# Kernel tuning notes

Measured on AMD Instinct MI355X. Metric: run time of the kernel, lower is better.

## Reference

```python
import jax, jax.numpy as jnp
import numpy as np

B, S, D = 8, 1024, 768
H, DH = 12, 64
FF = 3072
E = 8
CAP = 2 * (B * S) // E  # capacity per expert; routing of randn inputs never exceeds this
EPS = 1e-12


def layer_norm(x, g, b):
    mu = jnp.mean(x, axis=-1, keepdims=True)
    var = jnp.var(x, axis=-1, keepdims=True)
    return (x - mu) * jax.lax.rsqrt(var + EPS) * g + b


def setup_inputs() -> dict:
    key = jax.random.key(0)
    ks = jax.random.split(key, 16)
    sd = 0.02
    inp = {
        "hidden_states": jax.random.normal(ks[0], (B, S, D), jnp.float32),
        "attention_mask": jnp.zeros((B, 1, 1, S), jnp.float32),
        "Wq": jax.random.normal(ks[1], (D, D), jnp.float32) * sd,
        "bq": jnp.zeros((D,), jnp.float32),
        "Wk": jax.random.normal(ks[2], (D, D), jnp.float32) * sd,
        "bk": jnp.zeros((D,), jnp.float32),
        "Wv": jax.random.normal(ks[3], (D, D), jnp.float32) * sd,
        "bv": jnp.zeros((D,), jnp.float32),
        "Wo": jax.random.normal(ks[4], (D, D), jnp.float32) * sd,
        "bo": jnp.zeros((D,), jnp.float32),
        "ln1_g": jnp.ones((D,), jnp.float32),
        "ln1_b": jnp.zeros((D,), jnp.float32),
        "Wr": jax.random.normal(ks[5], (D, E), jnp.float32) * sd,
        "br": jnp.zeros((E,), jnp.float32),
        "W1": jax.random.normal(ks[6], (E, D, FF), jnp.float32) * sd,
        "b1": jnp.zeros((E, FF), jnp.float32),
        "W2": jax.random.normal(ks[7], (E, FF, D), jnp.float32) * sd,
        "b2": jnp.zeros((E, D), jnp.float32),
        "ln2_g": jnp.ones((D,), jnp.float32),
        "ln2_b": jnp.zeros((D,), jnp.float32),
    }
    return inp


def reference(hidden_states, attention_mask, Wq, bq, Wk, bk, Wv, bv, Wo, bo,
              ln1_g, ln1_b, Wr, br, W1, b1, W2, b2, ln2_g, ln2_b):
    x = hidden_states
    # ---- BERT self-attention (post-norm inside Attention) ----
    def heads(t):  # [B,S,D] -> [B,H,S,DH]
        return t.reshape(B, S, H, DH).transpose(0, 2, 1, 3)
    q = heads(x @ Wq + bq)
    k = heads(x @ Wk + bk)
    v = heads(x @ Wv + bv)
    scores = jnp.einsum('bhsd,bhtd->bhst', q, k) / jnp.sqrt(jnp.float32(DH))
    scores = scores + attention_mask  # additive mask, broadcast [B,1,1,S]
    probs = jax.nn.softmax(scores, axis=-1)
    ctx = jnp.einsum('bhst,bhtd->bhsd', probs, v)
    ctx = ctx.transpose(0, 2, 1, 3).reshape(B, S, D)
    att_output = layer_norm(x + (ctx @ Wo + bo), ln1_g, ln1_b)

    # ---- Switch (top-1) MoE FFN ----
    T = B * S
    xf = att_output.reshape(T, D)
    route = jax.nn.softmax(xf @ Wr + br, axis=-1)      # [T,E]
    gate = jnp.max(route, axis=-1)                      # [T]
    eidx = jnp.argmax(route, axis=-1)                   # [T]
    oh = jax.nn.one_hot(eidx, E, dtype=jnp.int32)       # [T,E]
    pos = (jnp.cumsum(oh, axis=0) * oh).sum(-1) - 1     # position within expert
    keep = (pos < CAP).astype(xf.dtype)                 # capacity drop mask
    p = jnp.clip(pos, 0, CAP - 1)
    # scatter tokens into per-expert buffers [E,CAP,D]
    buf = jnp.zeros((E, CAP, D), xf.dtype).at[eidx, p].add(xf * keep[:, None])
    h = jax.nn.gelu(jnp.einsum('ecd,edf->ecf', buf, W1) + b1[:, None, :], approximate=False)
    y = jnp.einsum('ecf,efd->ecd', h, W2) + b2[:, None, :]
    ffn = y[eidx, p] * (keep * gate)[:, None]            # gather + scale by route prob
    ffn_output = ffn.reshape(B, S, D)

    # dropout p=0 -> identity; post-norm residual
    return layer_norm(att_output + ffn_output, ln2_g, ln2_b)
```

## Files before the change

kernel.cpp:

```cpp
#include <hip/hip_runtime.h>
#include <hip/hip_bf16.h>
#include <math.h>

#define B_ 8
#define S_ 1024
#define D_ 768
#define H_ 12
#define DH_ 64
#define FF_ 3072
#define E_ 8
#define CAP_ 2048
#define T_ (B_ * S_)
#define QKVSTR 2304
#define QKSTR 1536

typedef __bf16 bf16_t;
typedef bf16_t bf16x8_t __attribute__((ext_vector_type(8)));
typedef bf16_t bf16x4_t __attribute__((ext_vector_type(4)));
typedef float floatx4_t __attribute__((ext_vector_type(4)));
typedef _Float16 f16_t;
typedef f16_t f16x8_t __attribute__((ext_vector_type(8)));
typedef f16_t f16x4_t __attribute__((ext_vector_type(4)));

#define LSTR 40

__global__ __launch_bounds__(256) void mfma_gemm_kernel(
    const bf16_t* __restrict__ Abase, const bf16_t* __restrict__ Btbase,
    const float* __restrict__ biasbase, bf16_t* __restrict__ Cbase,
    const int* __restrict__ cnt, int cnt_off,
    int M, int N, int K,
    long strideAz, long strideBz, long strideBiasz, long strideCz,
    int apply_gelu)
{
    __shared__ bf16_t As[128 * LSTR];
    __shared__ bf16_t Bs[128 * LSTR];
    const int z = blockIdx.z;
    const int row0 = blockIdx.y * 128;
    const int col0 = blockIdx.x * 128;
    if (cnt && row0 >= cnt[cnt_off + z]) return;
    const bf16_t* A  = Abase + (size_t)z * strideAz;
    const bf16_t* Bt = Btbase + (size_t)z * strideBz;
    const float* bias = biasbase + (size_t)z * strideBiasz;
    bf16_t* C = Cbase + (size_t)z * strideCz;

    const int tid = threadIdx.x;
    const int lane = tid & 63, wave = tid >> 6;
    const int wm = (wave >> 1) * 64, wn = (wave & 1) * 64;
    const int l16 = lane & 15, quad = lane >> 4;

    floatx4_t acc[4][4] = {};

    const int ch0 = tid, ch1 = tid + 256;
    const int r0a = ch0 >> 2, kc0 = (ch0 & 3) * 8;
    const int r1a = ch1 >> 2, kc1 = (ch1 & 3) * 8;

    for (int k0 = 0; k0 < K; k0 += 32) {
        __syncthreads();
        *(int4*)&As[r0a * LSTR + kc0] = *(const int4*)&A[(size_t)(row0 + r0a) * K + k0 + kc0];
        *(int4*)&As[r1a * LSTR + kc1] = *(const int4*)&A[(size_t)(row0 + r1a) * K + k0 + kc1];
        *(int4*)&Bs[r0a * LSTR + kc0] = *(const int4*)&Bt[(size_t)(col0 + r0a) * K + k0 + kc0];
        *(int4*)&Bs[r1a * LSTR + kc1] = *(const int4*)&Bt[(size_t)(col0 + r1a) * K + k0 + kc1];
        __syncthreads();
        bf16x8_t a[4], b[4];
        #pragma unroll
        for (int mt = 0; mt < 4; mt++)
            a[mt] = *(bf16x8_t*)&As[(wm + mt * 16 + l16) * LSTR + quad * 8];
        #pragma unroll
        for (int nt = 0; nt < 4; nt++)
            b[nt] = *(bf16x8_t*)&Bs[(wn + nt * 16 + l16) * LSTR + quad * 8];
        #pragma unroll
        for (int mt = 0; mt < 4; mt++)
            #pragma unroll
            for (int nt = 0; nt < 4; nt++)
                acc[mt][nt] = __builtin_amdgcn_mfma_f32_16x16x32_bf16(a[mt], b[nt], acc[mt][nt], 0, 0, 0);
    }

    #pragma unroll
    for (int mt = 0; mt < 4; mt++) {
        #pragma unroll
        for (int nt = 0; nt < 4; nt++) {
            const int col = col0 + wn + nt * 16 + l16;
            const float bv = bias[col];
            #pragma unroll
            for (int r = 0; r < 4; r++) {
                const int row = row0 + wm + mt * 16 + quad * 4 + r;
                float v = acc[mt][nt][r] + bv;
                if (apply_gelu) v = 0.5f * v * (1.0f + erff(v * 0.70710678118654752f));
                C[(size_t)row * N + col] = (bf16_t)v;
            }
        }
    }
}

__global__ __launch_bounds__(256) void mfma_split_gemm_kernel(
    const f16_t* __restrict__ Ah, const f16_t* __restrict__ Al,
    const f16_t* __restrict__ Bth, const f16_t* __restrict__ Btl,
    const float* __restrict__ bias0, const float* __restrict__ bias1,
    const float* __restrict__ bias2,
    float* __restrict__ C, int K, int N, int mode,
    f16_t* __restrict__ qkh, f16_t* __restrict__ qkl,
    f16_t* __restrict__ vth, f16_t* __restrict__ vtl)
{
    __shared__ f16_t Ash[128 * LSTR], Asl[128 * LSTR];
    __shared__ f16_t Bsh[128 * LSTR], Bsl[128 * LSTR];
    const int row0 = blockIdx.y * 128;
    const int col0 = blockIdx.x * 128;

    const int tid = threadIdx.x;
    const int lane = tid & 63, wave = tid >> 6;
    const int wm = (wave >> 1) * 64, wn = (wave & 1) * 64;
    const int l16 = lane & 15, quad = lane >> 4;

    floatx4_t acc[4][4] = {};

    const int r0a = tid >> 2, kc0 = (tid & 3) * 8;
    const int r1a = r0a + 64;

    for (int k0 = 0; k0 < K; k0 += 32) {
        __syncthreads();
        const size_t a0 = (size_t)(row0 + r0a) * K + k0 + kc0;
        const size_t a1 = (size_t)(row0 + r1a) * K + k0 + kc0;
        const size_t b0 = (size_t)(col0 + r0a) * K + k0 + kc0;
        const size_t b1 = (size_t)(col0 + r1a) * K + k0 + kc0;
        *(int4*)&Ash[r0a * LSTR + kc0] = *(const int4*)&Ah[a0];
        *(int4*)&Ash[r1a * LSTR + kc0] = *(const int4*)&Ah[a1];
        *(int4*)&Asl[r0a * LSTR + kc0] = *(const int4*)&Al[a0];
        *(int4*)&Asl[r1a * LSTR + kc0] = *(const int4*)&Al[a1];
        *(int4*)&Bsh[r0a * LSTR + kc0] = *(const int4*)&Bth[b0];
        *(int4*)&Bsh[r1a * LSTR + kc0] = *(const int4*)&Bth[b1];
        *(int4*)&Bsl[r0a * LSTR + kc0] = *(const int4*)&Btl[b0];
        *(int4*)&Bsl[r1a * LSTR + kc0] = *(const int4*)&Btl[b1];
        __syncthreads();
        f16x8_t bh[4], bl[4];
        #pragma unroll
        for (int nt = 0; nt < 4; nt++) {
            bh[nt] = *(f16x8_t*)&Bsh[(wn + nt * 16 + l16) * LSTR + quad * 8];
            bl[nt] = *(f16x8_t*)&Bsl[(wn + nt * 16 + l16) * LSTR + quad * 8];
        }
        #pragma unroll
        for (int mt = 0; mt < 4; mt++) {
            f16x8_t ah = *(f16x8_t*)&Ash[(wm + mt * 16 + l16) * LSTR + quad * 8];
            f16x8_t al = *(f16x8_t*)&Asl[(wm + mt * 16 + l16) * LSTR + quad * 8];
            #pragma unroll
            for (int nt = 0; nt < 4; nt++) {
                acc[mt][nt] = __builtin_amdgcn_mfma_f32_16x16x32_f16(ah, bh[nt], acc[mt][nt], 0, 0, 0);
                acc[mt][nt] = __builtin_amdgcn_mfma_f32_16x16x32_f16(al, bh[nt], acc[mt][nt], 0, 0, 0);
                acc[mt][nt] = __builtin_amdgcn_mfma_f32_16x16x32_f16(ah, bl[nt], acc[mt][nt], 0, 0, 0);
            }
        }
    }

    const int wsel = col0 / 768;
    const float* bias = (wsel == 0) ? bias0 : (wsel == 1) ? bias1 : bias2;
    const int colsub = col0 % 768;

    if (mode == 1) {
        if (col0 < 1536) {
            #pragma unroll
            for (int mt = 0; mt < 4; mt++) {
                #pragma unroll
                for (int nt = 0; nt < 4; nt++) {
                    const int col = col0 + wn + nt * 16 + l16;
                    const float bv = bias[colsub + wn + nt * 16 + l16];
                    #pragma unroll
                    for (int r = 0; r < 4; r++) {
                        const int row = row0 + wm + mt * 16 + quad * 4 + r;
                        float v = acc[mt][nt][r] * (1.0f / 64.0f) + bv;
                        f16_t hh = (f16_t)v;
                        const size_t o = (size_t)row * QKSTR + col;
                        qkh[o] = hh; qkl[o] = (f16_t)(v - (float)hh);
                    }
                }
            }
        } else {
            #pragma unroll
            for (int mt = 0; mt < 4; mt++) {
                const int rowb = row0 + wm + mt * 16 + quad * 4;
                const int bb = rowb >> 10, ss = rowb & 1023;
                #pragma unroll
                for (int nt = 0; nt < 4; nt++) {
                    const int d = (col0 - 1536) + wn + nt * 16 + l16;
                    const int hidx = d >> 6, dd = d & 63;
                    const float bv = bias[colsub + wn + nt * 16 + l16];
                    f16x4_t hv, lv;
                    #pragma unroll
                    for (int r = 0; r < 4; r++) {
                        float v = acc[mt][nt][r] * (1.0f / 64.0f) + bv;
                        hv[r] = (f16_t)v; lv[r] = (f16_t)(v - (float)hv[r]);
                    }
                    const size_t o = ((size_t)(bb * H_ + hidx) * DH_ + dd) * S_ + ss;
                    *(f16x4_t*)&vth[o] = hv;
                    *(f16x4_t*)&vtl[o] = lv;
                }
            }
        }
    } else {
        #pragma unroll
        for (int mt = 0; mt < 4; mt++) {
            #pragma unroll
            for (int nt = 0; nt < 4; nt++) {
                const int col = col0 + wn + nt * 16 + l16;
                const float bv = bias[colsub + wn + nt * 16 + l16];
                #pragma unroll
                for (int r = 0; r < 4; r++) {
                    const int row = row0 + wm + mt * 16 + quad * 4 + r;
                    C[(size_t)row * N + col] = acc[mt][nt][r] * (1.0f / 64.0f) + bv;
                }
            }
        }
    }
}

__global__ __launch_bounds__(256) void cast_split_kernel(
    const float* __restrict__ src, f16_t* __restrict__ hi, f16_t* __restrict__ lo)
{
    const int i = blockIdx.x * 256 + threadIdx.x;
    float4 v = ((const float4*)src)[i];
    const float vv[4] = {v.x, v.y, v.z, v.w};
    f16x4_t h, l;
    #pragma unroll
    for (int c = 0; c < 4; c++) {
        f16_t hh = (f16_t)vv[c];
        h[c] = hh; l[c] = (f16_t)(vv[c] - (float)hh);
    }
    ((f16x4_t*)hi)[i] = h;
    ((f16x4_t*)lo)[i] = l;
}

__global__ __launch_bounds__(256) void transpose_cast_split_kernel(
    const float* __restrict__ src, f16_t* __restrict__ dsth, f16_t* __restrict__ dstl,
    int R, int C)
{
    __shared__ float tile[32][33];
    const int r0 = blockIdx.y * 32, c0 = blockIdx.x * 32;
    const int tid = threadIdx.x;
    const int tr = tid >> 3, tc4 = (tid & 7) * 4;
    float4 v = *(const float4*)&src[(size_t)(r0 + tr) * C + c0 + tc4];
    tile[tr][tc4 + 0] = v.x * 64.0f; tile[tr][tc4 + 1] = v.y * 64.0f;
    tile[tr][tc4 + 2] = v.z * 64.0f; tile[tr][tc4 + 3] = v.w * 64.0f;
    __syncthreads();
    const int cc = tid >> 3, rr4 = (tid & 7) * 4;
    f16x4_t h, l;
    #pragma unroll
    for (int i = 0; i < 4; i++) {
        float f = tile[rr4 + i][cc];
        f16_t hh = (f16_t)f;
        h[i] = hh; l[i] = (f16_t)(f - (float)hh);
    }
    *(f16x4_t*)&dsth[(size_t)(c0 + cc) * R + r0 + rr4] = h;
    *(f16x4_t*)&dstl[(size_t)(c0 + cc) * R + r0 + rr4] = l;
}

__global__ __launch_bounds__(256) void transpose_cast_kernel(
    const float* __restrict__ src, bf16_t* __restrict__ dst, int R, int C)
{
    __shared__ float tile[32][33];
    const size_t zoff = (size_t)blockIdx.z * R * C;
    const float* s = src + zoff;
    bf16_t* d = dst + zoff;
    const int r0 = blockIdx.y * 32, c0 = blockIdx.x * 32;
    const int tid = threadIdx.x;
    const int tr = tid >> 3, tc4 = (tid & 7) * 4;
    float4 v = *(const float4*)&s[(size_t)(r0 + tr) * C + c0 + tc4];
    tile[tr][tc4 + 0] = v.x; tile[tr][tc4 + 1] = v.y;
    tile[tr][tc4 + 2] = v.z; tile[tr][tc4 + 3] = v.w;
    __syncthreads();
    const int cc = tid >> 3, rr4 = (tid & 7) * 4;
    bf16x4_t o;
    #pragma unroll
    for (int i = 0; i < 4; i++) o[i] = (bf16_t)tile[rr4 + i][cc];
    *(bf16x4_t*)&d[(size_t)(c0 + cc) * R + r0 + rr4] = o;
}

#define FSTR 72

__global__ __launch_bounds__(256) void flash_attn_mfma_kernel(
    const f16_t* __restrict__ qkh, const f16_t* __restrict__ qkl,
    const f16_t* __restrict__ vth, const f16_t* __restrict__ vtl,
    const float* __restrict__ mask,
    f16_t* __restrict__ ctxh, f16_t* __restrict__ ctxl)
{
    __shared__ f16_t Kh[64 * FSTR], Kl[64 * FSTR];
    __shared__ f16_t Vh[64 * FSTR], Vl[64 * FSTR];
    __shared__ f16_t Ph[64 * FSTR], Pl[64 * FSTR];
    const int flat = blockIdx.x;
    const int qt = (flat >> 3) & 15;
    const int p  = (flat & 7) + 8 * (flat >> 7);
    const int h = p % H_, b = p / H_;
    const int tid = threadIdx.x;
    const int lane = tid & 63, wave = tid >> 6;
    const int l16 = lane & 15, quad = lane >> 4;
    const int wm = wave * 16;
    const int q0 = qt * 64;
    const int pswz_w = quad << 3;
    const int quadr = quad ^ ((l16 >> 2) & 3);

    const size_t qoff = (size_t)(b * S_ + q0 + wm + l16) * QKSTR + h * DH_ + quad * 8;
    f16x8_t qh[2], ql[2];
    qh[0] = *(const f16x8_t*)&qkh[qoff];
    qh[1] = *(const f16x8_t*)&qkh[qoff + 32];
    ql[0] = *(const f16x8_t*)&qkl[qoff];
    ql[1] = *(const f16x8_t*)&qkl[qoff + 32];

    const int r0 = tid >> 3, s0 = (tid & 7) * 8;
    const int r1 = r0 + 32, s1 = s0;
    const size_t kbase = (size_t)b * S_ * QKSTR + 768 + (size_t)h * DH_;
    const size_t vbase = (size_t)(b * H_ + h) * DH_ * (size_t)S_;

    int4 kr0h, kr1h, kr0l, kr1l, vr0h, vr1h, vr0l, vr1l;
    auto prefetch = [&](int k0) {
        kr0h = *(const int4*)&qkh[kbase + (size_t)(k0 + r0) * QKSTR + s0];
        kr1h = *(const int4*)&qkh[kbase + (size_t)(k0 + r1) * QKSTR + s1];
        kr0l = *(const int4*)&qkl[kbase + (size_t)(k0 + r0) * QKSTR + s0];
        kr1l = *(const int4*)&qkl[kbase + (size_t)(k0 + r1) * QKSTR + s1];
        vr0h = *(const int4*)&vth[vbase + (size_t)r0 * S_ + k0 + s0];
        vr1h = *(const int4*)&vth[vbase + (size_t)r1 * S_ + k0 + s1];
        vr0l = *(const int4*)&vtl[vbase + (size_t)r0 * S_ + k0 + s0];
        vr1l = *(const int4*)&vtl[vbase + (size_t)r1 * S_ + k0 + s1];
    };
    prefetch(0);

    floatx4_t Oacc[4] = {};
    float mrun[4], lrun[4];
    #pragma unroll
    for (int i = 0; i < 4; i++) { mrun[i] = -1e30f; lrun[i] = 0.f; }

    for (int kt = 0; kt < S_ / 64; kt++) {
        __syncthreads();
        *(int4*)&Kh[r0 * FSTR + s0] = kr0h;
        *(int4*)&Kh[r1 * FSTR + s1] = kr1h;
        *(int4*)&Kl[r0 * FSTR + s0] = kr0l;
        *(int4*)&Kl[r1 * FSTR + s1] = kr1l;
        *(int4*)&Vh[r0 * FSTR + s0] = vr0h;
        *(int4*)&Vh[r1 * FSTR + s1] = vr1h;
        *(int4*)&Vl[r0 * FSTR + s0] = vr0l;
        *(int4*)&Vl[r1 * FSTR + s1] = vr1l;
        __syncthreads();
        if (kt + 1 < S_ / 64) prefetch((kt + 1) * 64);

        floatx4_t sacc[4] = {};
        __builtin_amdgcn_s_setprio(1);
        #pragma unroll
        for (int ks2 = 0; ks2 < 2; ks2++) {
            const f16x8_t ah = qh[ks2], al = ql[ks2];
            #pragma unroll
            for (int nt = 0; nt < 4; nt++) {
                f16x8_t bh = *(f16x8_t*)&Kh[(nt * 16 + l16) * FSTR + ks2 * 32 + quad * 8];
                f16x8_t bl = *(f16x8_t*)&Kl[(nt * 16 + l16) * FSTR + ks2 * 32 + quad * 8];
                sacc[nt] = __builtin_amdgcn_mfma_f32_16x16x32_f16(ah, bh, sacc[nt], 0, 0, 0);
                sacc[nt] = __builtin_amdgcn_mfma_f32_16x16x32_f16(al, bh, sacc[nt], 0, 0, 0);
                sacc[nt] = __builtin_amdgcn_mfma_f32_16x16x32_f16(ah, bl, sacc[nt], 0, 0, 0);
            }
        }
        __builtin_amdgcn_s_setprio(0);

        const int k0 = kt * 64;
        float mk[4];
        #pragma unroll
        for (int nt = 0; nt < 4; nt++) mk[nt] = mask[b * S_ + k0 + nt * 16 + l16];

        #pragma unroll
        for (int r = 0; r < 4; r++) {
            float s[4];
            float rmax = -1e30f;
            #pragma unroll
            for (int nt = 0; nt < 4; nt++) {
                s[nt] = sacc[nt][r] * 0.125f + mk[nt];
                rmax = fmaxf(rmax, s[nt]);
            }
            #pragma unroll
            for (int off = 1; off < 16; off <<= 1) rmax = fmaxf(rmax, __shfl_xor(rmax, off));
            if (rmax > mrun[r]) {
                const float alpha = __expf(mrun[r] - rmax);
                mrun[r] = rmax;
                lrun[r] *= alpha;
                #pragma unroll
                for (int nt = 0; nt < 4; nt++) Oacc[nt][r] *= alpha;
            }
            const float mnew = mrun[r];
            const int row = wm + quad * 4 + r;
            float rsum = 0.f;
            #pragma unroll
            for (int nt = 0; nt < 4; nt++) {
                float pv = __expf(s[nt] - mnew);
                f16_t ph = (f16_t)pv;
                const int csw = (nt * 16 + l16) ^ pswz_w;
                Ph[row * FSTR + csw] = ph;
                Pl[row * FSTR + csw] = (f16_t)(pv - (float)ph);
                rsum += pv;
            }
            #pragma unroll
            for (int off = 1; off < 16; off <<= 1) rsum += __shfl_xor(rsum, off);
            lrun[r] += rsum;
        }

        __builtin_amdgcn_s_setprio(1);
        #pragma unroll
        for (int ks2 = 0; ks2 < 2; ks2++) {
            f16x8_t ah = *(f16x8_t*)&Ph[(wm + l16) * FSTR + ks2 * 32 + quadr * 8];
            f16x8_t al = *(f16x8_t*)&Pl[(wm + l16) * FSTR + ks2 * 32 + quadr * 8];
            #pragma unroll
            for (int nt = 0; nt < 4; nt++) {
                f16x8_t bh = *(f16x8_t*)&Vh[(nt * 16 + l16) * FSTR + ks2 * 32 + quad * 8];
                f16x8_t bl = *(f16x8_t*)&Vl[(nt * 16 + l16) * FSTR + ks2 * 32 + quad * 8];
                Oacc[nt] = __builtin_amdgcn_mfma_f32_16x16x32_f16(ah, bh, Oacc[nt], 0, 0, 0);
                Oacc[nt] = __builtin_amdgcn_mfma_f32_16x16x32_f16(al, bh, Oacc[nt], 0, 0, 0);
                Oacc[nt] = __builtin_amdgcn_mfma_f32_16x16x32_f16(ah, bl, Oacc[nt], 0, 0, 0);
            }
        }
        __builtin_amdgcn_s_setprio(0);
    }

    float invl[4];
    #pragma unroll
    for (int r = 0; r < 4; r++) invl[r] = 1.0f / lrun[r];
    #pragma unroll
    for (int nt = 0; nt < 4; nt++) {
        #pragma unroll
        for (int r = 0; r < 4; r++) {
            const float v = Oacc[nt][r] * invl[r];
            const f16_t hh = (f16_t)v;
            const size_t o = (size_t)(b * S_ + q0 + wm + quad * 4 + r) * D_ + h * DH_ + nt * 16 + l16;
            ctxh[o] = hh;
            ctxl[o] = (f16_t)(v - (float)hh);
        }
    }
}

__global__ __launch_bounds__(256) void add_ln_kernel(
    const float* __restrict__ x, const float* __restrict__ y,
    const float* __restrict__ g, const float* __restrict__ bb,
    float* __restrict__ out)
{
    const int t = blockIdx.x;
    const int tid = threadIdx.x;
    __shared__ float red[256];
    float vals[3];
    float lsum = 0.f;
    #pragma unroll
    for (int i = 0; i < 3; i++) {
        int c = tid + i * 256;
        float v = x[(size_t)t * D_ + c] + y[(size_t)t * D_ + c];
        vals[i] = v; lsum += v;
    }
    red[tid] = lsum; __syncthreads();
    for (int off = 128; off > 0; off >>= 1) { if (tid < off) red[tid] += red[tid + off]; __syncthreads(); }
    const float mu = red[0] * (1.0f / D_);
    __syncthreads();
    float lvar = 0.f;
    #pragma unroll
    for (int i = 0; i < 3; i++) { float d = vals[i] - mu; lvar += d * d; }
    red[tid] = lvar; __syncthreads();
    for (int off = 128; off > 0; off >>= 1) { if (tid < off) red[tid] += red[tid + off]; __syncthreads(); }
    const float rstd = rsqrtf(red[0] * (1.0f / D_) + 1e-12f);
    #pragma unroll
    for (int i = 0; i < 3; i++) {
        int c = tid + i * 256;
        out[(size_t)t * D_ + c] = (vals[i] - mu) * rstd * g[c] + bb[c];
    }
}

__global__ __launch_bounds__(64) void router_kernel(
    const float* __restrict__ att, const float* __restrict__ Wr,
    const float* __restrict__ br, float* __restrict__ gate, int* __restrict__ eidx)
{
    const int t = blockIdx.x;
    const int lane = threadIdx.x;
    float lg[E_] = {};
    for (int d = lane; d < D_; d += 64) {
        float xv = att[(size_t)t * D_ + d];
        #pragma unroll
        for (int e = 0; e < E_; e++) lg[e] += xv * Wr[d * E_ + e];
    }
    #pragma unroll
    for (int off = 32; off > 0; off >>= 1)
        #pragma unroll
        for (int e = 0; e < E_; e++) lg[e] += __shfl_down(lg[e], off);
    if (lane == 0) {
        float mx = -1e30f; int mi = 0;
        #pragma unroll
        for (int e = 0; e < E_; e++) {
            lg[e] += br[e];
            if (lg[e] > mx) { mx = lg[e]; mi = e; }
        }
        float ssum = 0.f;
        #pragma unroll
        for (int e = 0; e < E_; e++) ssum += expf(lg[e] - mx);
        gate[t] = 1.0f / ssum;
        eidx[t] = mi;
    }
}

__global__ __launch_bounds__(256) void pos_scan_kernel(
    const int* __restrict__ eidx, const float* __restrict__ gate,
    int* __restrict__ pos, float* __restrict__ scale, int* __restrict__ cnt_out)
{
    __shared__ int cnt[256][E_];
    const int tid = threadIdx.x;
    const int start = tid * (T_ / 256);
    int lc[E_] = {};
    for (int i = 0; i < T_ / 256; i++) lc[eidx[start + i]]++;
    #pragma unroll
    for (int e = 0; e < E_; e++) cnt[tid][e] = lc[e];
    __syncthreads();
    if (tid < E_) {
        int run = 0;
        for (int i = 0; i < 256; i++) { int c = cnt[i][tid]; cnt[i][tid] = run; run += c; }
        cnt_out[tid] = run;
    }
    __syncthreads();
    int off[E_];
    #pragma unroll
    for (int e = 0; e < E_; e++) off[e] = cnt[tid][e];
    for (int i = 0; i < T_ / 256; i++) {
        int tk = start + i;
        int e = eidx[tk];
        int p = off[e]++;
        bool keep = p < CAP_;
        pos[tk] = p < CAP_ - 1 ? p : CAP_ - 1;
        scale[tk] = keep ? gate[tk] : 0.0f;
    }
}

__global__ __launch_bounds__(256) void scatter_kernel(
    const float* __restrict__ att, const int* __restrict__ eidx,
    const int* __restrict__ pos, const float* __restrict__ scale,
    bf16_t* __restrict__ buf)
{
    const int t = blockIdx.x;
    if (scale[t] == 0.0f) return;
    const int tid = threadIdx.x;
    const float* src = att + (size_t)t * D_;
    bf16_t* dst = buf + ((size_t)eidx[t] * CAP_ + pos[t]) * D_;
    for (int i = tid; i < D_; i += 256) dst[i] = (bf16_t)src[i];
}

__global__ __launch_bounds__(256) void final_ln_kernel(
    const float* __restrict__ att, const bf16_t* __restrict__ y,
    const int* __restrict__ eidx, const int* __restrict__ pos,
    const float* __restrict__ scale,
    const float* __restrict__ g, const float* __restrict__ bb,
    float* __restrict__ out)
{
    const int t = blockIdx.x;
    const int tid = threadIdx.x;
    __shared__ float red[256];
    const float sc = scale[t];
    const bf16_t* yrow = y + ((size_t)eidx[t] * CAP_ + pos[t]) * D_;
    float vals[3];
    float lsum = 0.f;
    #pragma unroll
    for (int i = 0; i < 3; i++) {
        int c = tid + i * 256;
        float v = att[(size_t)t * D_ + c] + (float)yrow[c] * sc;
        vals[i] = v; lsum += v;
    }
    red[tid] = lsum; __syncthreads();
    for (int off = 128; off > 0; off >>= 1) { if (tid < off) red[tid] += red[tid + off]; __syncthreads(); }
    const float mu = red[0] * (1.0f / D_);
    __syncthreads();
    float lvar = 0.f;
    #pragma unroll
    for (int i = 0; i < 3; i++) { float d = vals[i] - mu; lvar += d * d; }
    red[tid] = lvar; __syncthreads();
    for (int off = 128; off > 0; off >>= 1) { if (tid < off) red[tid] += red[tid + off]; __syncthreads(); }
    const float rstd = rsqrtf(red[0] * (1.0f / D_) + 1e-12f);
    #pragma unroll
    for (int i = 0; i < 3; i++) {
        int c = tid + i * 256;
        out[(size_t)t * D_ + c] = (vals[i] - mu) * rstd * g[c] + bb[c];
    }
}

extern "C" void kernel_launch(void* const* d_in, const int* in_sizes, int n_in,
                              void* d_out, int out_size, void* d_ws, size_t ws_size,
                              hipStream_t stream) {
    const float* x     = (const float*)d_in[0];
    const float* mask  = (const float*)d_in[1];
    const float* Wq    = (const float*)d_in[2];
    const float* bq    = (const float*)d_in[3];
    const float* Wk    = (const float*)d_in[4];
    const float* bk    = (const float*)d_in[5];
    const float* Wv    = (const float*)d_in[6];
    const float* bv    = (const float*)d_in[7];
    const float* Wo    = (const float*)d_in[8];
    const float* bo    = (const float*)d_in[9];
    const float* ln1g  = (const float*)d_in[10];
    const float* ln1b  = (const float*)d_in[11];
    const float* Wr    = (const float*)d_in[12];
    const float* br    = (const float*)d_in[13];
    const float* W1    = (const float*)d_in[14];
    const float* b1    = (const float*)d_in[15];
    const float* W2    = (const float*)d_in[16];
    const float* b2    = (const float*)d_in[17];
    const float* ln2g  = (const float*)d_in[18];
    const float* ln2b  = (const float*)d_in[19];
    float* out = (float*)d_out;

    char* ws = (char*)d_ws;
    const size_t TDB = (size_t)T_ * D_ * 4;
    f16_t* qkh  = (f16_t*)(ws);
    f16_t* qkl  = (f16_t*)(ws + TDB);
    f16_t* vth  = (f16_t*)(ws + 2 * TDB);
    f16_t* vtl  = (f16_t*)(ws + 2 * TDB + TDB / 2);
    f16_t* ctxh = (f16_t*)(ws + 3 * TDB);
    f16_t* ctxl = (f16_t*)(ws + 3 * TDB + TDB / 2);
    float* att_buf = (float*)(ws + 4 * TDB);
    f16_t* xh = (f16_t*)(ws + 3 * TDB);
    f16_t* xl = xh + (size_t)T_ * D_;
    f16_t* wqkvT_h = (f16_t*)(ws + 4 * TDB);
    f16_t* wqkvT_l = wqkvT_h + (size_t)QKVSTR * D_;
    f16_t* woT_h   = wqkvT_l + (size_t)QKVSTR * D_;
    f16_t* woT_l   = woT_h + (size_t)D_ * D_;
    float* proj_b = (float*)(ws);
    bf16_t* W1T = (bf16_t*)(ws);
    bf16_t* W2T = (bf16_t*)(ws + (size_t)E_ * FF_ * D_ * 2);
    bf16_t* h_b = (bf16_t*)(ws + (size_t)2 * E_ * FF_ * D_ * 2);
    char*  smallp  = ws + 5 * TDB;
    float* gate_b  = (float*)(smallp);
    int*   eidx_b  = (int*)(smallp + 32768);
    int*   pos_b   = (int*)(smallp + 2 * 32768);
    float* scale_b = (float*)(smallp + 3 * 32768);
    int*   cnt_b   = (int*)(smallp + 4 * 32768);
    bf16_t* buf_b  = (bf16_t*)(smallp + 4 * 32768 + 128);
    bf16_t* y_b    = (bf16_t*)((char*)buf_b + (size_t)E_ * CAP_ * D_ * 2);
    bf16_t* h8_b   = (bf16_t*)((char*)y_b + (size_t)E_ * CAP_ * D_ * 2);
    const size_t need8 = ((char*)h8_b - ws) + (size_t)E_ * CAP_ * FF_ * 2;

    dim3 blk(256);
    cast_split_kernel<<<dim3(T_ * D_ / 1024), blk, 0, stream>>>(x, xh, xl);
    transpose_cast_split_kernel<<<dim3(D_ / 32, D_ / 32), blk, 0, stream>>>(
        Wq, wqkvT_h, wqkvT_l, D_, D_);
    transpose_cast_split_kernel<<<dim3(D_ / 32, D_ / 32), blk, 0, stream>>>(
        Wk, wqkvT_h + (size_t)D_ * D_, wqkvT_l + (size_t)D_ * D_, D_, D_);
    transpose_cast_split_kernel<<<dim3(D_ / 32, D_ / 32), blk, 0, stream>>>(
        Wv, wqkvT_h + (size_t)2 * D_ * D_, wqkvT_l + (size_t)2 * D_ * D_, D_, D_);
    transpose_cast_split_kernel<<<dim3(D_ / 32, D_ / 32), blk, 0, stream>>>(
        Wo, woT_h, woT_l, D_, D_);
    mfma_split_gemm_kernel<<<dim3(QKVSTR / 128, T_ / 128), blk, 0, stream>>>(
        xh, xl, wqkvT_h, wqkvT_l, bq, bk, bv, nullptr, D_, QKVSTR,
        1, qkh, qkl, vth, vtl);
    flash_attn_mfma_kernel<<<dim3((S_ / 64) * H_ * B_), blk, 0, stream>>>(
        qkh, qkl, vth, vtl, mask, ctxh, ctxl);
    mfma_split_gemm_kernel<<<dim3(D_ / 128, T_ / 128), blk, 0, stream>>>(
        ctxh, ctxl, woT_h, woT_l, bo, bo, bo, proj_b, D_, D_,
        0, nullptr, nullptr, nullptr, nullptr);
    add_ln_kernel<<<dim3(T_), blk, 0, stream>>>(x, proj_b, ln1g, ln1b, att_buf);
    router_kernel<<<dim3(T_), dim3(64), 0, stream>>>(att_buf, Wr, br, gate_b, eidx_b);
    pos_scan_kernel<<<dim3(1), blk, 0, stream>>>(eidx_b, gate_b, pos_b, scale_b, cnt_b);
    transpose_cast_kernel<<<dim3(FF_ / 32, D_ / 32, E_), blk, 0, stream>>>(W1, W1T, D_, FF_);
    transpose_cast_kernel<<<dim3(D_ / 32, FF_ / 32, E_), blk, 0, stream>>>(W2, W2T, FF_, D_);
    hipMemsetAsync(buf_b, 0, (size_t)E_ * CAP_ * D_ * 2, stream);
    scatter_kernel<<<dim3(T_), blk, 0, stream>>>(att_buf, eidx_b, pos_b, scale_b, buf_b);
    if (ws_size >= need8) {
        mfma_gemm_kernel<<<dim3(FF_ / 128, CAP_ / 128, E_), blk, 0, stream>>>(
            buf_b, W1T, b1, h8_b,
            cnt_b, 0, CAP_, FF_, D_,
            (long)CAP_ * D_, (long)FF_ * D_, (long)FF_, (long)CAP_ * FF_, 1);
        mfma_gemm_kernel<<<dim3(D_ / 128, CAP_ / 128, E_), blk, 0, stream>>>(
            h8_b, W2T, b2, y_b,
            cnt_b, 0, CAP_, D_, FF_,
            (long)CAP_ * FF_, (long)D_ * FF_, (long)D_, (long)CAP_ * D_, 0);
    } else {
        for (int bch = 0; bch < 4; bch++) {
            const int e0 = bch * 2;
            mfma_gemm_kernel<<<dim3(FF_ / 128, CAP_ / 128, 2), blk, 0, stream>>>(
                buf_b + (size_t)e0 * CAP_ * D_, W1T + (size_t)e0 * FF_ * D_,
                b1 + (size_t)e0 * FF_, h_b,
                cnt_b, e0, CAP_, FF_, D_,
                (long)CAP_ * D_, (long)FF_ * D_, (long)FF_, (long)CAP_ * FF_, 1);
            mfma_gemm_kernel<<<dim3(D_ / 128, CAP_ / 128, 2), blk, 0, stream>>>(
                h_b, W2T + (size_t)e0 * D_ * FF_,
                b2 + (size_t)e0 * D_, y_b + (size_t)e0 * CAP_ * D_,
                cnt_b, e0, CAP_, D_, FF_,
                (long)CAP_ * FF_, (long)D_ * FF_, (long)D_, (long)CAP_ * D_, 0);
        }
    }
    final_ln_kernel<<<dim3(T_), blk, 0, stream>>>(att_buf, y_b, eidx_b, pos_b, scale_b, ln2g, ln2b, out);
}
```

Measured before the change: 842.7 us.

## Halve flash-attention KV tile to 32 keys and raise occupancy

```diff
diff --git a/kernel.cpp b/kernel.cpp
--- a/kernel.cpp
+++ b/kernel.cpp
@@ -272,17 +272,20 @@
     *(bf16x4_t*)&d[(size_t)(c0 + cc) * R + r0 + rr4] = o;
 }
 
-#define FSTR 72
-
-__global__ __launch_bounds__(256) void flash_attn_mfma_kernel(
+#define KVB 32
+#define KSTR 72
+#define VSTR 40
+#define PSTR 40
+
+__global__ __launch_bounds__(256, 5) void flash_attn_mfma_kernel(
     const f16_t* __restrict__ qkh, const f16_t* __restrict__ qkl,
     const f16_t* __restrict__ vth, const f16_t* __restrict__ vtl,
     const float* __restrict__ mask,
     f16_t* __restrict__ ctxh, f16_t* __restrict__ ctxl)
 {
-    __shared__ f16_t Kh[64 * FSTR], Kl[64 * FSTR];
-    __shared__ f16_t Vh[64 * FSTR], Vl[64 * FSTR];
-    __shared__ f16_t Ph[64 * FSTR], Pl[64 * FSTR];
+    __shared__ f16_t Kh[KVB * KSTR], Kl[KVB * KSTR];
+    __shared__ f16_t Vh[DH_ * VSTR], Vl[DH_ * VSTR];
+    __shared__ f16_t Ph[64 * PSTR],  Pl[64 * PSTR];
     const int flat = blockIdx.x;
     const int qt = (flat >> 3) & 15;
     const int p  = (flat & 7) + 8 * (flat >> 7);
@@ -292,8 +295,6 @@
     const int l16 = lane & 15, quad = lane >> 4;
     const int wm = wave * 16;
     const int q0 = qt * 64;
-    const int pswz_w = quad << 3;
-    const int quadr = quad ^ ((l16 >> 2) & 3);
 
     const size_t qoff = (size_t)(b * S_ + q0 + wm + l16) * QKSTR + h * DH_ + quad * 8;
     f16x8_t qh[2], ql[2];
@@ -302,21 +303,24 @@
     ql[0] = *(const f16x8_t*)&qkl[qoff];
     ql[1] = *(const f16x8_t*)&qkl[qoff + 32];
 
-    const int r0 = tid >> 3, s0 = (tid & 7) * 8;
-    const int r1 = r0 + 32, s1 = s0;
+    const int stv = tid >> 7;
+    const int t7 = tid & 127;
+    const int krow = t7 >> 2, kcol = (t7 & 3) * 16;
+    const int vrow = t7 >> 1, vcol = (t7 & 1) * 16;
     const size_t kbase = (size_t)b * S_ * QKSTR + 768 + (size_t)h * DH_;
     const size_t vbase = (size_t)(b * H_ + h) * DH_ * (size_t)S_;
 
-    int4 kr0h, kr1h, kr0l, kr1l, vr0h, vr1h, vr0l, vr1l;
+    int4 pr0h, pr1h, pr0l, pr1l;
     auto prefetch = [&](int k0) {
-        kr0h = *(const int4*)&qkh[kbase + (size_t)(k0 + r0) * QKSTR + s0];
-        kr1h = *(const int4*)&qkh[kbase + (size_t)(k0 + r1) * QKSTR + s1];
-        kr0l = *(const int4*)&qkl[kbase + (size_t)(k0 + r0) * QKSTR + s0];
-        kr1l = *(const int4*)&qkl[kbase + (size_t)(k0 + r1) * QKSTR + s1];
-        vr0h = *(const int4*)&vth[vbase + (size_t)r0 * S_ + k0 + s0];
-        vr1h = *(const int4*)&vth[vbase + (size_t)r1 * S_ + k0 + s1];
-        vr0l = *(const int4*)&vtl[vbase + (size_t)r0 * S_ + k0 + s0];
-        vr1l = *(const int4*)&vtl[vbase + (size_t)r1 * S_ + k0 + s1];
+        if (stv == 0) {
+            const size_t g = kbase + (size_t)(k0 + krow) * QKSTR + kcol;
+            pr0h = *(const int4*)&qkh[g]; pr1h = *(const int4*)&qkh[g + 8];
+            pr0l = *(const int4*)&qkl[g]; pr1l = *(const int4*)&qkl[g + 8];
+        } else {
+            const size_t g = vbase + (size_t)vrow * S_ + k0 + vcol;
+            pr0h = *(const int4*)&vth[g]; pr1h = *(const int4*)&vth[g + 8];
+            pr0l = *(const int4*)&vtl[g]; pr1l = *(const int4*)&vtl[g + 8];
+        }
     };
     prefetch(0);
 
@@ -325,28 +329,31 @@
     #pragma unroll
     for (int i = 0; i < 4; i++) { mrun[i] = -1e30f; lrun[i] = 0.f; }
 
-    for (int kt = 0; kt < S_ / 64; kt++) {
+    for (int kt = 0; kt < S_ / KVB; kt++) {
         __syncthreads();
-        *(int4*)&Kh[r0 * FSTR + s0] = kr0h;
-        *(int4*)&Kh[r1 * FSTR + s1] = kr1h;
-        *(int4*)&Kl[r0 * FSTR + s0] = kr0l;
-        *(int4*)&Kl[r1 * FSTR + s1] = kr1l;
-        *(int4*)&Vh[r0 * FSTR + s0] = vr0h;
-        *(int4*)&Vh[r1 * FSTR + s1] = vr1h;
-        *(int4*)&Vl[r0 * FSTR + s0] = vr0l;
-        *(int4*)&Vl[r1 * FSTR + s1] = vr1l;
+        if (stv == 0) {
+            f16_t* dh_ = &Kh[krow * KSTR + kcol];
+            f16_t* dl_ = &Kl[krow * KSTR + kcol];
+            *(int4*)dh_ = pr0h; *(int4*)(dh_ + 8) = pr1h;
+            *(int4*)dl_ = pr0l; *(int4*)(dl_ + 8) = pr1l;
+        } else {
+            f16_t* dh_ = &Vh[vrow * VSTR + vcol];
+            f16_t* dl_ = &Vl[vrow * VSTR + vcol];
+            *(int4*)dh_ = pr0h; *(int4*)(dh_ + 8) = pr1h;
+            *(int4*)dl_ = pr0l; *(int4*)(dl_ + 8) = pr1l;
+        }
         __syncthreads();
-        if (kt + 1 < S_ / 64) prefetch((kt + 1) * 64);
-
-        floatx4_t sacc[4] = {};
+        if (kt + 1 < S_ / KVB) prefetch((kt + 1) * KVB);
+
+        floatx4_t sacc[2] = {};
         __builtin_amdgcn_s_setprio(1);
         #pragma unroll
         for (int ks2 = 0; ks2 < 2; ks2++) {
             const f16x8_t ah = qh[ks2], al = ql[ks2];
             #pragma unroll
-            for (int nt = 0; nt < 4; nt++) {
-                f16x8_t bh = *(f16x8_t*)&Kh[(nt * 16 + l16) * FSTR + ks2 * 32 + quad * 8];
-                f16x8_t bl = *(f16x8_t*)&Kl[(nt * 16 + l16) * FSTR + ks2 * 32 + quad * 8];
+            for (int nt = 0; nt < 2; nt++) {
+                f16x8_t bh = *(f16x8_t*)&Kh[(nt * 16 + l16) * KSTR + ks2 * 32 + quad * 8];
+                f16x8_t bl = *(f16x8_t*)&Kl[(nt * 16 + l16) * KSTR + ks2 * 32 + quad * 8];
                 sacc[nt] = __builtin_amdgcn_mfma_f32_16x16x32_f16(ah, bh, sacc[nt], 0, 0, 0);
                 sacc[nt] = __builtin_amdgcn_mfma_f32_16x16x32_f16(al, bh, sacc[nt], 0, 0, 0);
                 sacc[nt] = __builtin_amdgcn_mfma_f32_16x16x32_f16(ah, bl, sacc[nt], 0, 0, 0);
@@ -354,59 +361,49 @@
         }
         __builtin_amdgcn_s_setprio(0);
 
-        const int k0 = kt * 64;
-        float mk[4];
-        #pragma unroll
-        for (int nt = 0; nt < 4; nt++) mk[nt] = mask[b * S_ + k0 + nt * 16 + l16];
+        const int k0 = kt * KVB;
+        float mk[2];
+        #pragma unroll
+        for (int nt = 0; nt < 2; nt++) mk[nt] = mask[b * S_ + k0 + nt * 16 + l16];
 
         #pragma unroll
         for (int r = 0; r < 4; r++) {
-            float s[4];
-            float rmax = -1e30f;
-            #pragma unroll
-            for (int nt = 0; nt < 4; nt++) {
-                s[nt] = sacc[nt][r] * 0.125f + mk[nt];
-                rmax = fmaxf(rmax, s[nt]);
+            float s0 = sacc[0][r] * 0.125f + mk[0];
+            float s1 = sacc[1][r] * 0.125f + mk[1];
+            float rmax = fmaxf(s0, s1);
+            #pragma unroll
+            for (int off = 1; off < 16; off <<= 1) rmax = fmaxf(rmax, __shfl_xor(rmax, off));
+            const float mnew = fmaxf(mrun[r], rmax);
+            const float alpha = __expf(mrun[r] - mnew);
+            mrun[r] = mnew;
+            const int row = wm + quad * 4 + r;
+            float p0 = __expf(s0 - mnew);
+            float p1 = __expf(s1 - mnew);
+            f16_t p0h = (f16_t)p0, p1h = (f16_t)p1;
+            Ph[row * PSTR + l16] = p0h;
+            Pl[row * PSTR + l16] = (f16_t)(p0 - (float)p0h);
+            Ph[row * PSTR + 16 + l16] = p1h;
+            Pl[row * PSTR + 16 + l16] = (f16_t)(p1 - (float)p1h);
+            float rsum = p0 + p1;
+            #pragma unroll
+            for (int off = 1; off < 16; off <<= 1) rsum += __shfl_xor(rsum, off);
+            lrun[r] = lrun[r] * alpha + rsum;
+            #pragma unroll
+            for (int nt2 = 0; nt2 < 4; nt2++) Oacc[nt2][r] *= alpha;
+        }
+
+        __builtin_amdgcn_s_setprio(1);
+        {
+            f16x8_t pah = *(f16x8_t*)&Ph[(wm + l16) * PSTR + quad * 8];
+            f16x8_t pal = *(f16x8_t*)&Pl[(wm + l16) * PSTR + quad * 8];
+            #pragma unroll
+            for (int nt2 = 0; nt2 < 4; nt2++) {
+                f16x8_t bh = *(f16x8_t*)&Vh[(nt2 * 16 + l16) * VSTR + quad * 8];
+                f16x8_t bl = *(f16x8_t*)&Vl[(nt2 * 16 + l16) * VSTR + quad * 8];
+                Oacc[nt2] = __builtin_amdgcn_mfma_f32_16x16x32_f16(pah, bh, Oacc[nt2], 0, 0, 0);
+                Oacc[nt2] = __builtin_amdgcn_mfma_f32_16x16x32_f16(pal, bh, Oacc[nt2], 0, 0, 0);
+                Oacc[nt2] = __builtin_amdgcn_mfma_f32_16x16x32_f16(pah, bl, Oacc[nt2], 0, 0, 0);
             }
-            #pragma unroll
-            for (int off = 1; off < 16; off <<= 1) rmax = fmaxf(rmax, __shfl_xor(rmax, off));
-            if (rmax > mrun[r]) {
-                const float alpha = __expf(mrun[r] - rmax);
-                mrun[r] = rmax;
-                lrun[r] *= alpha;
-                #pragma unroll
-                for (int nt = 0; nt < 4; nt++) Oacc[nt][r] *= alpha;
-            }
-            const float mnew = mrun[r];
-            const int row = wm + quad * 4 + r;
-            float rsum = 0.f;
-            #pragma unroll
-            for (int nt = 0; nt < 4; nt++) {
-                float pv = __expf(s[nt] - mnew);
-                f16_t ph = (f16_t)pv;
-                const int csw = (nt * 16 + l16) ^ pswz_w;
-                Ph[row * FSTR + csw] = ph;
-                Pl[row * FSTR + csw] = (f16_t)(pv - (float)ph);
-                rsum += pv;
-            }
-            #pragma unroll
-            for (int off = 1; off < 16; off <<= 1) rsum += __shfl_xor(rsum, off);
-            lrun[r] += rsum;
-        }
-
-        __builtin_amdgcn_s_setprio(1);
-        #pragma unroll
-        for (int ks2 = 0; ks2 < 2; ks2++) {
-            f16x8_t ah = *(f16x8_t*)&Ph[(wm + l16) * FSTR + ks2 * 32 + quadr * 8];
-            f16x8_t al = *(f16x8_t*)&Pl[(wm + l16) * FSTR + ks2 * 32 + quadr * 8];
-            #pragma unroll
-            for (int nt = 0; nt < 4; nt++) {
-                f16x8_t bh = *(f16x8_t*)&Vh[(nt * 16 + l16) * FSTR + ks2 * 32 + quad * 8];
-                f16x8_t bl = *(f16x8_t*)&Vl[(nt * 16 + l16) * FSTR + ks2 * 32 + quad * 8];
-                Oacc[nt] = __builtin_amdgcn_mfma_f32_16x16x32_f16(ah, bh, Oacc[nt], 0, 0, 0);
-                Oacc[nt] = __builtin_amdgcn_mfma_f32_16x16x32_f16(al, bh, Oacc[nt], 0, 0, 0);
-                Oacc[nt] = __builtin_amdgcn_mfma_f32_16x16x32_f16(ah, bl, Oacc[nt], 0, 0, 0);
-            }
         }
         __builtin_amdgcn_s_setprio(0);
     }
@@ -415,12 +412,12 @@
     #pragma unroll
     for (int r = 0; r < 4; r++) invl[r] = 1.0f / lrun[r];
     #pragma unroll
-    for (int nt = 0; nt < 4; nt++) {
+    for (int nt2 = 0; nt2 < 4; nt2++) {
         #pragma unroll
         for (int r = 0; r < 4; r++) {
-            const float v = Oacc[nt][r] * invl[r];
+            const float v = Oacc[nt2][r] * invl[r];
             const f16_t hh = (f16_t)v;
-            const size_t o = (size_t)(b * S_ + q0 + wm + quad * 4 + r) * D_ + h * DH_ + nt * 16 + l16;
+            const size_t o = (size_t)(b * S_ + q0 + wm + quad * 4 + r) * D_ + h * DH_ + nt2 * 16 + l16;
             ctxh[o] = hh;
             ctxl[o] = (f16_t)(v - (float)hh);
         }
```

New measurement: 881.3 us. +4.6%, slower.

## Compute softmax row sums via MFMA ones column and drop branchy rescale

Applied to the files above, without the earlier changes.

```diff
diff --git a/kernel.cpp b/kernel.cpp
--- a/kernel.cpp
+++ b/kernel.cpp
@@ -281,7 +281,7 @@
     f16_t* __restrict__ ctxh, f16_t* __restrict__ ctxl)
 {
     __shared__ f16_t Kh[64 * FSTR], Kl[64 * FSTR];
-    __shared__ f16_t Vh[64 * FSTR], Vl[64 * FSTR];
+    __shared__ f16_t Vh[80 * FSTR], Vl[80 * FSTR];
     __shared__ f16_t Ph[64 * FSTR], Pl[64 * FSTR];
     const int flat = blockIdx.x;
     const int qt = (flat >> 3) & 15;
@@ -292,8 +292,6 @@
     const int l16 = lane & 15, quad = lane >> 4;
     const int wm = wave * 16;
     const int q0 = qt * 64;
-    const int pswz_w = quad << 3;
-    const int quadr = quad ^ ((l16 >> 2) & 3);
 
     const size_t qoff = (size_t)(b * S_ + q0 + wm + l16) * QKSTR + h * DH_ + quad * 8;
     f16x8_t qh[2], ql[2];
@@ -301,6 +299,14 @@
     qh[1] = *(const f16x8_t*)&qkh[qoff + 32];
     ql[0] = *(const f16x8_t*)&qkl[qoff];
     ql[1] = *(const f16x8_t*)&qkl[qoff + 32];
+
+    #pragma unroll
+    for (int i = 0; i < 4; i++) {
+        int idx = i * 256 + tid;
+        int rr = 64 + (idx >> 6), cc = idx & 63;
+        Vh[rr * FSTR + cc] = (rr == 64) ? (f16_t)1.0f : (f16_t)0.0f;
+        Vl[rr * FSTR + cc] = (f16_t)0.0f;
+    }
 
     const int r0 = tid >> 3, s0 = (tid & 7) * 8;
     const int r1 = r0 + 32, s1 = s0;
@@ -320,10 +326,10 @@
     };
     prefetch(0);
 
-    floatx4_t Oacc[4] = {};
-    float mrun[4], lrun[4];
-    #pragma unroll
-    for (int i = 0; i < 4; i++) { mrun[i] = -1e30f; lrun[i] = 0.f; }
+    floatx4_t Oacc[5] = {};
+    float mrun[4];
+    #pragma unroll
+    for (int i = 0; i < 4; i++) mrun[i] = -1e30f;
 
     for (int kt = 0; kt < S_ / 64; kt++) {
         __syncthreads();
@@ -370,42 +376,35 @@
             }
             #pragma unroll
             for (int off = 1; off < 16; off <<= 1) rmax = fmaxf(rmax, __shfl_xor(rmax, off));
-            if (rmax > mrun[r]) {
-                const float alpha = __expf(mrun[r] - rmax);
-                mrun[r] = rmax;
-                lrun[r] *= alpha;
-                #pragma unroll
-                for (int nt = 0; nt < 4; nt++) Oacc[nt][r] *= alpha;
-            }
-            const float mnew = mrun[r];
+            const float mnew = fmaxf(mrun[r], rmax);
+            const float alpha = __expf(mrun[r] - mnew);
+            mrun[r] = mnew;
             const int row = wm + quad * 4 + r;
-            float rsum = 0.f;
             #pragma unroll
             for (int nt = 0; nt < 4; nt++) {
                 float pv = __expf(s[nt] - mnew);
                 f16_t ph = (f16_t)pv;
-                const int csw = (nt * 16 + l16) ^ pswz_w;
-                Ph[row * FSTR + csw] = ph;
-                Pl[row * FSTR + csw] = (f16_t)(pv - (float)ph);
-                rsum += pv;
-            }
-            #pragma unroll
-            for (int off = 1; off < 16; off <<= 1) rsum += __shfl_xor(rsum, off);
-            lrun[r] += rsum;
+                Ph[row * FSTR + nt * 16 + l16] = ph;
+                Pl[row * FSTR + nt * 16 + l16] = (f16_t)(pv - (float)ph);
+            }
+            #pragma unroll
+            for (int nt = 0; nt < 5; nt++) Oacc[nt][r] *= alpha;
         }
 
         __builtin_amdgcn_s_setprio(1);
         #pragma unroll
         for (int ks2 = 0; ks2 < 2; ks2++) {
-            f16x8_t ah = *(f16x8_t*)&Ph[(wm + l16) * FSTR + ks2 * 32 + quadr * 8];
-            f16x8_t al = *(f16x8_t*)&Pl[(wm + l16) * FSTR + ks2 * 32 + quadr * 8];
-            #pragma unroll
-            for (int nt = 0; nt < 4; nt++) {
+            f16x8_t ah = *(f16x8_t*)&Ph[(wm + l16) * FSTR + ks2 * 32 + quad * 8];
+            f16x8_t al = *(f16x8_t*)&Pl[(wm + l16) * FSTR + ks2 * 32 + quad * 8];
+            #pragma unroll
+            for (int nt = 0; nt < 5; nt++) {
                 f16x8_t bh = *(f16x8_t*)&Vh[(nt * 16 + l16) * FSTR + ks2 * 32 + quad * 8];
-                f16x8_t bl = *(f16x8_t*)&Vl[(nt * 16 + l16) * FSTR + ks2 * 32 + quad * 8];
                 Oacc[nt] = __builtin_amdgcn_mfma_f32_16x16x32_f16(ah, bh, Oacc[nt], 0, 0, 0);
                 Oacc[nt] = __builtin_amdgcn_mfma_f32_16x16x32_f16(al, bh, Oacc[nt], 0, 0, 0);
-                Oacc[nt] = __builtin_amdgcn_mfma_f32_16x16x32_f16(ah, bl, Oacc[nt], 0, 0, 0);
+                if (nt < 4) {
+                    f16x8_t bl = *(f16x8_t*)&Vl[(nt * 16 + l16) * FSTR + ks2 * 32 + quad * 8];
+                    Oacc[nt] = __builtin_amdgcn_mfma_f32_16x16x32_f16(ah, bl, Oacc[nt], 0, 0, 0);
+                }
             }
         }
         __builtin_amdgcn_s_setprio(0);
@@ -413,7 +412,10 @@
 
     float invl[4];
     #pragma unroll
-    for (int r = 0; r < 4; r++) invl[r] = 1.0f / lrun[r];
+    for (int r = 0; r < 4; r++) {
+        const float lsum = __shfl(Oacc[4][r], lane & 48);
+        invl[r] = 1.0f / lsum;
+    }
     #pragma unroll
     for (int nt = 0; nt < 4; nt++) {
         #pragma unroll
```

Measured after the change: 816.3 us. 1.03x faster.
